# Kernel tuning notes

Measured on AMD Instinct MI355X. Metric: run time of the kernel, lower is better.

Reference implementation:

```python
import jax, jax.numpy as jnp
import numpy as np

NUM_GRAPHS = 256


def _mean_aggregate(h, src, dst, num_nodes):
    # DGL copy_src + mean reduce: dst node gets mean of src-node features over in-edges.
    summed = jax.ops.segment_sum(h[src], dst, num_segments=num_nodes)  # [N, F]
    deg = jax.ops.segment_sum(jnp.ones((src.shape[0],), h.dtype), dst, num_segments=num_nodes)
    return summed / jnp.maximum(deg, 1.0)[:, None]


def setup_inputs() -> dict:
    key = jax.random.key(0)
    ks = jax.random.split(key, 10)
    N, E, D_IN, H1, H2, OUT = 50000, 800000, 128, 256, 128, 1
    s = lambda fan: 1.0 / np.sqrt(fan)
    return {
        "h": jax.random.normal(ks[0], (N, D_IN), jnp.float32),
        "src": jax.random.randint(ks[1], (E,), 0, N),
        "dst": jax.random.randint(ks[2], (E,), 0, N),
        "graph_ids": jnp.sort(jax.random.randint(ks[3], (N,), 0, NUM_GRAPHS)),
        "W1": jax.random.normal(ks[4], (D_IN, H1), jnp.float32) * s(D_IN),
        "b1": jnp.zeros((H1,), jnp.float32),
        "W2": jax.random.normal(ks[5], (H1, H1), jnp.float32) * s(H1),
        "b2": jnp.zeros((H1,), jnp.float32),
        "Wr1": jax.random.normal(ks[6], (H1, H2), jnp.float32) * s(H1),
        "br1": jnp.zeros((H2,), jnp.float32),
        "Wr2": jax.random.normal(ks[7], (H2, OUT), jnp.float32) * s(H2),
        "br2": jnp.zeros((OUT,), jnp.float32),
    }


def reference(h, src, dst, graph_ids, W1, b1, W2, b2, Wr1, br1, Wr2, br2):
    N = h.shape[0]
    # GCN layer 1: mean-aggregate then linear+ReLU
    h = _mean_aggregate(h, src, dst, N)
    h = jax.nn.relu(h @ W1 + b1)
    # GCN layer 2
    h = _mean_aggregate(h, src, dst, N)
    h = jax.nn.relu(h @ W2 + b2)
    # dgl.mean_nodes readout: per-graph mean of node features
    gsum = jax.ops.segment_sum(h, graph_ids, num_segments=NUM_GRAPHS)  # [G, H1]
    gcnt = jax.ops.segment_sum(jnp.ones((N,), h.dtype), graph_ids, num_segments=NUM_GRAPHS)
    hg = gsum / jnp.maximum(gcnt, 1.0)[:, None]
    hidden = hg @ Wr1 + br1
    return hidden @ Wr2 + br2  # [G, 1]
```

## Files before the change

kernel.cpp:

```cpp
#include <hip/hip_runtime.h>


#define NUM_GRAPHS 256

#define CNT_B0 0
#define CNT_NB 1024
#define CST_B0 (CNT_B0 + CNT_NB)
#define CST_NB 512
#define GST_B0 (CST_B0 + CST_NB)
#define GST_NB 64
#define WT1_B0 (GST_B0 + GST_NB)
#define WT1_NB 16
#define WT2_B0 (WT1_B0 + WT1_NB)
#define WT2_NB 32
#define MISC_NB (WT2_B0 + WT2_NB)

typedef __attribute__((ext_vector_type(8))) short bf16x8;
typedef __attribute__((ext_vector_type(4))) float f32x4;

__device__ inline unsigned short f2bf(float f) {
    unsigned u = __float_as_uint(f);
    return (unsigned short)((u + 0x7fff + ((u >> 16) & 1)) >> 16);
}
__device__ inline float bflo(unsigned u) { return __uint_as_float(u << 16); }
__device__ inline float bfhi(unsigned u) { return __uint_as_float(u & 0xffff0000u); }


__launch_bounds__(256)
__global__ void misc_kernel(const int* __restrict__ dst, const int* __restrict__ gids,
                            const float* __restrict__ h,
                            const float* __restrict__ W1, const float* __restrict__ W2,
                            int* __restrict__ cnt, unsigned short* __restrict__ rank,
                            int* __restrict__ gstart,
                            unsigned short* __restrict__ hb,
                            unsigned short* __restrict__ Wt1, unsigned short* __restrict__ Wt2,
                            int N, int E) {
    int b = blockIdx.x, tid = threadIdx.x;
    if (b < CST_B0) {
        int lid = (b - CNT_B0) * 256 + tid;
        for (int e = lid; e < E; e += CNT_NB * 256) {
            int d = __builtin_nontemporal_load(&dst[e]);
            int r = atomicAdd(&cnt[d], 1);
            __builtin_nontemporal_store((unsigned short)r, &rank[e]);
        }
    } else if (b < GST_B0) {
        int lid = (b - CST_B0) * 256 + tid;
        int total4 = N * 32;
        for (int i = lid; i < total4; i += CST_NB * 256) {
            float4 v = *(const float4*)(h + (size_t)i * 4);
            ushort4 o;
            o.x = f2bf(v.x); o.y = f2bf(v.y); o.z = f2bf(v.z); o.w = f2bf(v.w);
            *(ushort4*)(hb + (size_t)i * 4) = o;
        }
    } else if (b < WT1_B0) {
        int lid = (b - GST_B0) * 256 + tid;
        for (int n = lid; n < N; n += GST_NB * 256) {
            int g = gids[n];
            int gp = (n == 0) ? -1 : gids[n - 1];
            for (int x = gp + 1; x <= g; ++x) gstart[x] = n;
            if (n == N - 1)
                for (int x = g + 1; x <= NUM_GRAPHS; ++x) gstart[x] = N;
        }
    } else if (b < WT2_B0) {
        int lid = (b - WT1_B0) * 256 + tid;
        for (int i = lid; i < 256 * 128; i += WT1_NB * 256)
            Wt1[i] = f2bf(W1[(size_t)(i & 127) * 256 + (i >> 7)]);
    } else {
        int lid = (b - WT2_B0) * 256 + tid;
        for (int i = lid; i < 256 * 256; i += WT2_NB * 256)
            Wt2[i] = f2bf(W2[(size_t)(i & 255) * 256 + (i >> 8)]);
    }
}


__global__ void scan_kernel(const int* __restrict__ cnt, int* __restrict__ offs,
                            int* __restrict__ pval, int* __restrict__ pflag,
                            int N, int E) {
    __shared__ int wsum[16];
    __shared__ int sbase;
    int tid = threadIdx.x;
    int lane = tid & 63;
    int wid = tid >> 6;
    int b = blockIdx.x;
    int i = b * 1024 + tid;
    int v = (i < N) ? cnt[i] : 0;
    int x = v;
    #pragma unroll
    for (int d = 1; d < 64; d <<= 1) {
        int y = __shfl_up(x, d, 64);
        if (lane >= d) x += y;
    }
    if (lane == 63) wsum[wid] = x;
    __syncthreads();
    if (wid == 0) {
        int s = (lane < 16) ? wsum[lane] : 0;
        #pragma unroll
        for (int d = 1; d < 16; d <<= 1) {
            int y = __shfl_up(s, d, 64);
            if (lane >= d) s += y;
        }
        if (lane < 16) wsum[lane] = s;
    }
    __syncthreads();
    int wbase = (wid > 0) ? wsum[wid - 1] : 0;
    int ex = wbase + x - v;

    if (tid == 1023) {
        pval[b] = wbase + x;
        __threadfence();
        atomicExch(&pflag[b], 1);
    }
    if (wid == 0) {
        int sum = 0;
        if (lane < b) {
            while (atomicAdd(&pflag[lane], 0) == 0) {}
            sum = atomicAdd(&pval[lane], 0);
        }
        #pragma unroll
        for (int d = 32; d > 0; d >>= 1) sum += __shfl_xor(sum, d, 64);
        if (lane == 0) sbase = sum;
    }
    __syncthreads();
    if (i < N) offs[i] = sbase + ex;
    if (b == 0 && tid == 0) offs[N] = E;
}


__global__ void scatter_kernel(const int* __restrict__ src, const int* __restrict__ dst,
                               const int* __restrict__ offs,
                               const unsigned short* __restrict__ rank,
                               unsigned short* __restrict__ eidx, int E) {
    int e = blockIdx.x * blockDim.x + threadIdx.x;
    if (e < E) {
        int d = __builtin_nontemporal_load(&dst[e]);
        unsigned short r = __builtin_nontemporal_load(&rank[e]);
        int s = __builtin_nontemporal_load(&src[e]);
        eidx[offs[d] + (int)r] = (unsigned short)s;
    }
}


template <int D>
__global__ void agg_mean_bf16_kernel(const unsigned short* __restrict__ feat,
                                     const int* __restrict__ offs,
                                     const unsigned short* __restrict__ eidx,
                                     unsigned short* __restrict__ out, int N) {
    constexpr int VPL = D / 64;
    int wave = blockIdx.x * (blockDim.x >> 6) + (threadIdx.x >> 6);
    int lane = threadIdx.x & 63;
    if (wave >= N) return;
    int beg = offs[wave], end = offs[wave + 1];
    float acc[VPL];
    #pragma unroll
    for (int i = 0; i < VPL; ++i) acc[i] = 0.0f;

    int j = beg;
    for (; j + 8 <= end; j += 8) {
        int s[8];
        #pragma unroll
        for (int u = 0; u < 8; ++u) s[u] = (int)eidx[j + u];
        if constexpr (VPL == 2) {
            unsigned v[8];
            #pragma unroll
            for (int u = 0; u < 8; ++u)
                v[u] = *(const unsigned*)(feat + (size_t)s[u] * D + lane * 2);
            #pragma unroll
            for (int u = 0; u < 8; ++u) { acc[0] += bflo(v[u]); acc[1] += bfhi(v[u]); }
        } else {
            uint2 v[8];
            #pragma unroll
            for (int u = 0; u < 8; ++u)
                v[u] = *(const uint2*)(feat + (size_t)s[u] * D + lane * 4);
            #pragma unroll
            for (int u = 0; u < 8; ++u) {
                acc[0] += bflo(v[u].x); acc[1] += bfhi(v[u].x);
                acc[2] += bflo(v[u].y); acc[3] += bfhi(v[u].y);
            }
        }
    }
    for (; j < end; ++j) {
        int s = (int)eidx[j];
        if constexpr (VPL == 2) {
            unsigned v = *(const unsigned*)(feat + (size_t)s * D + lane * 2);
            acc[0] += bflo(v); acc[1] += bfhi(v);
        } else {
            uint2 v = *(const uint2*)(feat + (size_t)s * D + lane * 4);
            acc[0] += bflo(v.x); acc[1] += bfhi(v.x);
            acc[2] += bflo(v.y); acc[3] += bfhi(v.y);
        }
    }

    int deg = end - beg;
    float invd = 1.0f / (float)(deg > 0 ? deg : 1);
    unsigned short* orow = out + (size_t)wave * D + lane * VPL;
    if constexpr (VPL == 2) {
        ushort2 o; o.x = f2bf(acc[0] * invd); o.y = f2bf(acc[1] * invd);
        *(ushort2*)orow = o;
    } else {
        ushort4 o;
        o.x = f2bf(acc[0] * invd); o.y = f2bf(acc[1] * invd);
        o.z = f2bf(acc[2] * invd); o.w = f2bf(acc[3] * invd);
        *(ushort4*)orow = o;
    }
}


template <int K, int MODE>
__launch_bounds__(256)
__global__ void gemm_mfma_kernel(const unsigned short* __restrict__ A,
                                 const unsigned short* __restrict__ Wt,
                                 const float* __restrict__ bias,
                                 unsigned short* __restrict__ Cb,
                                 const int* __restrict__ gids,
                                 float* __restrict__ gsum,
                                 int N) {
    constexpr int LDS = 40;
    __shared__ unsigned short As[64 * LDS];
    __shared__ unsigned short Bs[256 * LDS];

    int tid = threadIdx.x;
    int wave = tid >> 6;
    int lane = tid & 63;
    int m = lane & 15;
    int q = lane >> 4;
    int rowBase = blockIdx.x * 64;

    f32x4 acc[4][4] = {};

    for (int kc = 0; kc < K; kc += 32) {
        {
            int r = tid >> 2;
            int seg = tid & 3;
            int gr = rowBase + r;
            uint4 v = make_uint4(0, 0, 0, 0);
            if (gr < N) v = *(const uint4*)(A + (size_t)gr * K + kc + seg * 8);
            *(uint4*)&As[r * LDS + seg * 8] = v;
        }
        #pragma unroll
        for (int it = 0; it < 4; ++it) {
            int n = (tid >> 2) + it * 64;
            int seg = tid & 3;
            uint4 v = *(const uint4*)(Wt + (size_t)n * K + kc + seg * 8);
            *(uint4*)&Bs[n * LDS + seg * 8] = v;
        }
        __syncthreads();

        bf16x8 af[4], bfr[4];
        #pragma unroll
        for (int r = 0; r < 4; ++r)
            af[r] = *(const bf16x8*)&As[(r * 16 + m) * LDS + q * 8];
        #pragma unroll
        for (int c = 0; c < 4; ++c)
            bfr[c] = *(const bf16x8*)&Bs[(wave * 64 + c * 16 + m) * LDS + q * 8];
        #pragma unroll
        for (int r = 0; r < 4; ++r)
            #pragma unroll
            for (int c = 0; c < 4; ++c)
                acc[r][c] = __builtin_amdgcn_mfma_f32_16x16x32_bf16(af[r], bfr[c], acc[r][c], 0, 0, 0);
        __syncthreads();
    }

    if constexpr (MODE == 0) {
        #pragma unroll
        for (int c = 0; c < 4; ++c) {
            int col = wave * 64 + c * 16 + m;
            float bv = bias[col];
            #pragma unroll
            for (int r = 0; r < 4; ++r) {
                #pragma unroll
                for (int reg = 0; reg < 4; ++reg) {
                    int grow = rowBase + r * 16 + q * 4 + reg;
                    if (grow < N)
                        Cb[(size_t)grow * 256 + col] = f2bf(fmaxf(acc[r][c][reg] + bv, 0.0f));
                }
            }
        }
    } else {
        int* sgid = (int*)As;
        if (tid < 64) {
            int gr = rowBase + tid;
            sgid[tid] = (gr < N) ? gids[gr] : -1;
        }
        __syncthreads();
        #pragma unroll
        for (int c = 0; c < 4; ++c) {
            int col = wave * 64 + c * 16 + m;
            float bv = bias[col];
            float partsum = 0.0f;
            int gprev = -1;
            #pragma unroll
            for (int r = 0; r < 4; ++r) {
                #pragma unroll
                for (int reg = 0; reg < 4; ++reg) {
                    int lr = r * 16 + q * 4 + reg;
                    if (rowBase + lr < N) {
                        int g = sgid[lr];
                        float o = fmaxf(acc[r][c][reg] + bv, 0.0f);
                        if (g != gprev) {
                            if (gprev >= 0) atomicAdd(&gsum[gprev * 256 + col], partsum);
                            partsum = 0.0f;
                            gprev = g;
                        }
                        partsum += o;
                    }
                }
            }
            if (gprev >= 0) atomicAdd(&gsum[gprev * 256 + col], partsum);
        }
    }
}


__global__ void final_kernel(const float* __restrict__ gsum, const int* __restrict__ gstart,
                             const float* __restrict__ Wr1, const float* __restrict__ br1,
                             const float* __restrict__ Wr2, const float* __restrict__ br2,
                             float* __restrict__ out) {
    int g = blockIdx.x;
    int j = threadIdx.x;
    int c = gstart[g + 1] - gstart[g];
    float invc = 1.0f / (float)(c > 0 ? c : 1);
    const float* gs = gsum + g * 256;
    float acc = br1[j];
    for (int k = 0; k < 256; ++k)
        acc += (gs[k] * invc) * Wr1[k * 128 + j];
    float p = acc * Wr2[j];
    #pragma unroll
    for (int d = 32; d > 0; d >>= 1) p += __shfl_down(p, d, 64);
    __shared__ float ws2[2];
    if ((j & 63) == 0) ws2[j >> 6] = p;
    __syncthreads();
    if (j == 0) out[g] = ws2[0] + ws2[1] + br2[0];
}


extern "C" void kernel_launch(void* const* d_in, const int* in_sizes, int n_in,
                              void* d_out, int out_size, void* d_ws, size_t ws_size,
                              hipStream_t stream) {
    const float* h    = (const float*)d_in[0];
    const int*   src  = (const int*)d_in[1];
    const int*   dst  = (const int*)d_in[2];
    const int*   gids = (const int*)d_in[3];
    const float* W1   = (const float*)d_in[4];
    const float* b1   = (const float*)d_in[5];
    const float* W2   = (const float*)d_in[6];
    const float* b2   = (const float*)d_in[7];
    const float* Wr1  = (const float*)d_in[8];
    const float* br1  = (const float*)d_in[9];
    const float* Wr2  = (const float*)d_in[10];
    const float* br2  = (const float*)d_in[11];

    int N = in_sizes[0] / 128;
    int E = in_sizes[1];
    int nScanBlocks = (N + 1023) / 1024;

    char* w = (char*)d_ws;
    unsigned short* hb     = (unsigned short*)w;  w += (size_t)N * 128 * sizeof(unsigned short);
    unsigned short* h1b    = (unsigned short*)w;  w += (size_t)N * 256 * sizeof(unsigned short);
    unsigned short* aggOut = (unsigned short*)w;  w += (size_t)N * 256 * sizeof(unsigned short);
    int* cnt    = (int*)w;              w += (size_t)N * sizeof(int);
    float* gsum = (float*)w;            w += (size_t)NUM_GRAPHS * 256 * sizeof(float);
    int* pflag  = (int*)w;              w += 64 * sizeof(int);
    int* pval   = (int*)w;              w += 64 * sizeof(int);
    int* offs   = (int*)w;              w += (size_t)(N + 1) * sizeof(int);
    unsigned short* eidx = (unsigned short*)w;  w += (size_t)E * sizeof(unsigned short);
    unsigned short* rank = (unsigned short*)w;  w += (size_t)E * sizeof(unsigned short);
    unsigned short* Wt1 = (unsigned short*)w;   w += 256 * 128 * sizeof(unsigned short);
    unsigned short* Wt2 = (unsigned short*)w;   w += 256 * 256 * sizeof(unsigned short);
    int* gstart = (int*)w;              w += (size_t)(NUM_GRAPHS + 1) * sizeof(int);

    hipMemsetAsync(cnt, 0,
                   (size_t)N * sizeof(int) + (size_t)NUM_GRAPHS * 256 * sizeof(float) +
                   64 * sizeof(int),
                   stream);
    misc_kernel<<<MISC_NB, 256, 0, stream>>>(dst, gids, h, W1, W2, cnt, rank, gstart,
                                             hb, Wt1, Wt2, N, E);
    scan_kernel<<<nScanBlocks, 1024, 0, stream>>>(cnt, offs, pval, pflag, N, E);
    scatter_kernel<<<(E + 255) / 256, 256, 0, stream>>>(src, dst, offs, rank, eidx, E);

    agg_mean_bf16_kernel<128><<<(N + 3) / 4, 256, 0, stream>>>(hb, offs, eidx, aggOut, N);
    gemm_mfma_kernel<128, 0><<<(N + 63) / 64, 256, 0, stream>>>(aggOut, Wt1, b1, h1b, nullptr, nullptr, N);

    agg_mean_bf16_kernel<256><<<(N + 3) / 4, 256, 0, stream>>>(h1b, offs, eidx, aggOut, N);
    gemm_mfma_kernel<256, 1><<<(N + 63) / 64, 256, 0, stream>>>(aggOut, Wt2, b2, nullptr, gids, gsum, N);

    final_kernel<<<NUM_GRAPHS, 128, 0, stream>>>(gsum, gstart, Wr1, br1, Wr2, br2, (float*)d_out);
}
```

Measured before the change: 315.4 us.

## Pack scan flag into value, reduce readout atomics across lanes, split final GEMV

```diff
diff --git a/kernel.cpp b/kernel.cpp
--- a/kernel.cpp
+++ b/kernel.cpp
@@ -105,16 +105,14 @@
     int wbase = (wid > 0) ? wsum[wid - 1] : 0;
     int ex = wbase + x - v;
 
-    if (tid == 1023) {
-        pval[b] = wbase + x;
-        __threadfence();
-        atomicExch(&pflag[b], 1);
-    }
+    if (tid == 1023)
+        atomicExch(&pval[b], (wbase + x) | 0x40000000);
     if (wid == 0) {
         int sum = 0;
         if (lane < b) {
-            while (atomicAdd(&pflag[lane], 0) == 0) {}
-            sum = atomicAdd(&pval[lane], 0);
+            int pv;
+            do { pv = atomicAdd(&pval[lane], 0); } while (!(pv & 0x40000000));
+            sum = pv & 0x3fffffff;
         }
         #pragma unroll
         for (int d = 32; d > 0; d >>= 1) sum += __shfl_xor(sum, d, 64);
@@ -123,6 +121,7 @@
     __syncthreads();
     if (i < N) offs[i] = sbase + ex;
     if (b == 0 && tid == 0) offs[N] = E;
+    (void)pflag;
 }
 
 
@@ -279,33 +278,33 @@
         int* sgid = (int*)As;
         if (tid < 64) {
             int gr = rowBase + tid;
-            sgid[tid] = (gr < N) ? gids[gr] : -1;
+            sgid[tid] = (gr < N) ? gids[gr] : 0x7fffffff;
         }
         __syncthreads();
+        int lastValid = N - 1 - rowBase;
+        if (lastValid > 63) lastValid = 63;
+        int gmin = sgid[0];
+        int gmax = sgid[lastValid];
         #pragma unroll
         for (int c = 0; c < 4; ++c) {
             int col = wave * 64 + c * 16 + m;
             float bv = bias[col];
-            float partsum = 0.0f;
-            int gprev = -1;
-            #pragma unroll
-            for (int r = 0; r < 4; ++r) {
+            for (int g = gmin; g <= gmax; ++g) {
+                float p = 0.0f;
                 #pragma unroll
-                for (int reg = 0; reg < 4; ++reg) {
-                    int lr = r * 16 + q * 4 + reg;
-                    if (rowBase + lr < N) {
-                        int g = sgid[lr];
-                        float o = fmaxf(acc[r][c][reg] + bv, 0.0f);
-                        if (g != gprev) {
-                            if (gprev >= 0) atomicAdd(&gsum[gprev * 256 + col], partsum);
-                            partsum = 0.0f;
-                            gprev = g;
-                        }
-                        partsum += o;
+                for (int r = 0; r < 4; ++r) {
+                    #pragma unroll
+                    for (int reg = 0; reg < 4; ++reg) {
+                        int lr = r * 16 + q * 4 + reg;
+                        if (sgid[lr] == g)
+                            p += fmaxf(acc[r][c][reg] + bv, 0.0f);
                     }
                 }
+                p += __shfl_xor(p, 16, 64);
+                p += __shfl_xor(p, 32, 64);
+                if (q == 0 && p != 0.0f)
+                    atomicAdd(&gsum[g * 256 + col], p);
             }
-            if (gprev >= 0) atomicAdd(&gsum[gprev * 256 + col], partsum);
         }
     }
 }
@@ -315,21 +314,30 @@
                              const float* __restrict__ Wr1, const float* __restrict__ br1,
                              const float* __restrict__ Wr2, const float* __restrict__ br2,
                              float* __restrict__ out) {
+    __shared__ float part[512];
+    __shared__ float ws2[2];
     int g = blockIdx.x;
-    int j = threadIdx.x;
+    int t = threadIdx.x;
+    int j = t & 127;
+    int kq = t >> 7;
     int c = gstart[g + 1] - gstart[g];
     float invc = 1.0f / (float)(c > 0 ? c : 1);
     const float* gs = gsum + g * 256;
-    float acc = br1[j];
-    for (int k = 0; k < 256; ++k)
-        acc += (gs[k] * invc) * Wr1[k * 128 + j];
-    float p = acc * Wr2[j];
-    #pragma unroll
-    for (int d = 32; d > 0; d >>= 1) p += __shfl_down(p, d, 64);
-    __shared__ float ws2[2];
-    if ((j & 63) == 0) ws2[j >> 6] = p;
-    __syncthreads();
-    if (j == 0) out[g] = ws2[0] + ws2[1] + br2[0];
+    float acc = 0.0f;
+    #pragma unroll 8
+    for (int k = kq * 64; k < kq * 64 + 64; ++k)
+        acc += gs[k] * Wr1[k * 128 + j];
+    part[t] = acc;
+    __syncthreads();
+    if (t < 128) {
+        float s = part[j] + part[128 + j] + part[256 + j] + part[384 + j];
+        float p = (s * invc + br1[j]) * Wr2[j];
+        #pragma unroll
+        for (int d = 32; d > 0; d >>= 1) p += __shfl_down(p, d, 64);
+        if ((t & 63) == 0) ws2[t >> 6] = p;
+    }
+    __syncthreads();
+    if (t == 0) out[g] = ws2[0] + ws2[1] + br2[0];
 }
 
 
@@ -370,7 +378,7 @@
 
     hipMemsetAsync(cnt, 0,
                    (size_t)N * sizeof(int) + (size_t)NUM_GRAPHS * 256 * sizeof(float) +
-                   64 * sizeof(int),
+                   128 * sizeof(int),
                    stream);
     misc_kernel<<<MISC_NB, 256, 0, stream>>>(dst, gids, h, W1, W2, cnt, rank, gstart,
                                              hb, Wt1, Wt2, N, E);
@@ -383,5 +391,5 @@
     agg_mean_bf16_kernel<256><<<(N + 3) / 4, 256, 0, stream>>>(h1b, offs, eidx, aggOut, N);
     gemm_mfma_kernel<256, 1><<<(N + 63) / 64, 256, 0, stream>>>(aggOut, Wt2, b2, nullptr, gids, gsum, N);
 
-    final_kernel<<<NUM_GRAPHS, 128, 0, stream>>>(gsum, gstart, Wr1, br1, Wr2, br2, (float*)d_out);
-}
+    final_kernel<<<NUM_GRAPHS, 512, 0, stream>>>(gsum, gstart, Wr1, br1, Wr2, br2, (float*)d_out);
+}
```

After: 301.7 us. -4.3%, faster.
